# Optimization experiments

Hardware: AMD Instinct MI355X
Metric: run time of the kernel (lower is better)

## Reference

```python
import jax, jax.numpy as jnp
import numpy as np

EPS = 1e-12  # tf.nn.l2_normalize epsilon used by keras Dot(normalize=True)

def setup_inputs() -> dict:
    key = jax.random.key(0)
    k1, k2 = jax.random.split(key)
    a = jax.random.normal(k1, (16, 4096, 256), dtype=jnp.float32)
    b = jax.random.normal(k2, (16, 4096, 256), dtype=jnp.float32)
    return {"a": a, "b": b}

def _l2_normalize(x, axis=-1):
    # matches tf.nn.l2_normalize: x * rsqrt(max(sum(x^2), eps))
    sq = jnp.sum(x * x, axis=axis, keepdims=True)
    return x * jax.lax.rsqrt(jnp.maximum(sq, EPS))

def reference(a, b):
    # Original: full [B,N,N] cosine-similarity matrix then diag_part.
    # The diagonal equals the rowwise cosine similarity, computed directly.
    an = _l2_normalize(a, axis=2)  # [B, N, D]
    bn = _l2_normalize(b, axis=2)  # [B, N, D]
    return jnp.sum(an * bn, axis=2)  # [B, N]
```

## Files before the change

### kernel.cpp

```cpp
#include <hip/hip_runtime.h>


#define D 256
#define EPS 1e-12f

__global__ __launch_bounds__(256) void cosine_rows_kernel(
    const float* __restrict__ a,
    const float* __restrict__ b,
    float* __restrict__ out,
    int n_rows)
{
    const int lane = threadIdx.x & 63;
    const int wave = threadIdx.x >> 6;
    const int sub  = lane & 15;
    const int grp  = lane >> 4;
    const int row  = blockIdx.x * 16 + wave * 4 + grp;
    if (row >= n_rows) return;

    const float4* a4 = reinterpret_cast<const float4*>(a + (size_t)row * D);
    const float4* b4 = reinterpret_cast<const float4*>(b + (size_t)row * D);

    float4 av0 = a4[sub];
    float4 av1 = a4[sub + 16];
    float4 av2 = a4[sub + 32];
    float4 av3 = a4[sub + 48];
    float4 bv0 = b4[sub];
    float4 bv1 = b4[sub + 16];
    float4 bv2 = b4[sub + 32];
    float4 bv3 = b4[sub + 48];

    float sa = 0.f, sb = 0.f, sab = 0.f;
    #define ACC(av, bv)                                          \
        sa  += av.x*av.x + av.y*av.y + av.z*av.z + av.w*av.w;    \
        sb  += bv.x*bv.x + bv.y*bv.y + bv.z*bv.z + bv.w*bv.w;    \
        sab += av.x*bv.x + av.y*bv.y + av.z*bv.z + av.w*bv.w;
    ACC(av0, bv0)
    ACC(av1, bv1)
    ACC(av2, bv2)
    ACC(av3, bv3)
    #undef ACC

    #pragma unroll
    for (int off = 8; off > 0; off >>= 1) {
        sa  += __shfl_xor(sa,  off, 16);
        sb  += __shfl_xor(sb,  off, 16);
        sab += __shfl_xor(sab, off, 16);
    }

    if (sub == 0) {
        out[row] = sab * rsqrtf(fmaxf(sa, EPS)) * rsqrtf(fmaxf(sb, EPS));
    }
}

extern "C" void kernel_launch(void* const* d_in, const int* in_sizes, int n_in,
                              void* d_out, int out_size, void* d_ws, size_t ws_size,
                              hipStream_t stream)
{
    const float* a = (const float*)d_in[0];
    const float* b = (const float*)d_in[1];
    float* out = (float*)d_out;

    const int n_rows = out_size;
    const int rows_per_block = 16;
    const int grid = (n_rows + rows_per_block - 1) / rows_per_block;

    cosine_rows_kernel<<<grid, 256, 0, stream>>>(a, b, out, n_rows);
}
```

Baseline: 141.3 us.

## Split cosine row reduction into partial-sum and shuffle-reduce kernels

Splits the single fused kernel into two launches. The first computes per-thread partial sums of a·a, b·b and a·b and writes them to workspace. The second reloads those partials, does the 16-lane shuffle reduction and writes the normalized dot product. This adds a second launch plus an extra write and read of three partial arrays (3×16 floats per row), probably to test whether separating the reduction helps. The accumulation also switches to explicit fmaf chains.

```diff
diff --git a/kernel.cpp b/kernel.cpp
--- a/kernel.cpp
+++ b/kernel.cpp
@@ -1,44 +1,58 @@
 #include <hip/hip_runtime.h>
 
 
-#define D 256
 #define EPS 1e-12f
 
-__global__ __launch_bounds__(256) void cosine_rows_kernel(
-    const float* __restrict__ a,
-    const float* __restrict__ b,
-    float* __restrict__ out,
-    int n_rows)
+__global__ __launch_bounds__(256) void cosine_phase1(
+    const float4* __restrict__ a4,
+    const float4* __restrict__ b4,
+    float* __restrict__ ws_sa,
+    float* __restrict__ ws_sb,
+    float* __restrict__ ws_sab,
+    int n_part)
 {
-    const int lane = threadIdx.x & 63;
-    const int wave = threadIdx.x >> 6;
-    const int sub  = lane & 15;
-    const int grp  = lane >> 4;
-    const int row  = blockIdx.x * 16 + wave * 4 + grp;
-    if (row >= n_rows) return;
+    const int g = blockIdx.x * 256 + threadIdx.x;
+    if (g >= n_part) return;
+    const int row = g >> 4;
+    const int sub = g & 15;
 
-    const float4* a4 = reinterpret_cast<const float4*>(a + (size_t)row * D);
-    const float4* b4 = reinterpret_cast<const float4*>(b + (size_t)row * D);
+    const float4* __restrict__ ar = a4 + (size_t)row * 64 + sub;
+    const float4* __restrict__ br = b4 + (size_t)row * 64 + sub;
 
-    float4 av0 = a4[sub];
-    float4 av1 = a4[sub + 16];
-    float4 av2 = a4[sub + 32];
-    float4 av3 = a4[sub + 48];
-    float4 bv0 = b4[sub];
-    float4 bv1 = b4[sub + 16];
-    float4 bv2 = b4[sub + 32];
-    float4 bv3 = b4[sub + 48];
+    float4 av0 = ar[0],  av1 = ar[16], av2 = ar[32], av3 = ar[48];
+    float4 bv0 = br[0],  bv1 = br[16], bv2 = br[32], bv3 = br[48];
 
     float sa = 0.f, sb = 0.f, sab = 0.f;
-    #define ACC(av, bv)                                          \
-        sa  += av.x*av.x + av.y*av.y + av.z*av.z + av.w*av.w;    \
-        sb  += bv.x*bv.x + bv.y*bv.y + bv.z*bv.z + bv.w*bv.w;    \
-        sab += av.x*bv.x + av.y*bv.y + av.z*bv.z + av.w*bv.w;
+    #define ACC(av, bv)                                                       \
+        sa  = fmaf(av.x, av.x, fmaf(av.y, av.y, fmaf(av.z, av.z, fmaf(av.w, av.w, sa))));   \
+        sb  = fmaf(bv.x, bv.x, fmaf(bv.y, bv.y, fmaf(bv.z, bv.z, fmaf(bv.w, bv.w, sb))));   \
+        sab = fmaf(av.x, bv.x, fmaf(av.y, bv.y, fmaf(av.z, bv.z, fmaf(av.w, bv.w, sab))));
     ACC(av0, bv0)
     ACC(av1, bv1)
     ACC(av2, bv2)
     ACC(av3, bv3)
     #undef ACC
+
+    ws_sa[g]  = sa;
+    ws_sb[g]  = sb;
+    ws_sab[g] = sab;
+}
+
+__global__ __launch_bounds__(256) void cosine_phase2(
+    const float* __restrict__ ws_sa,
+    const float* __restrict__ ws_sb,
+    const float* __restrict__ ws_sab,
+    float* __restrict__ out,
+    int n_part)
+{
+    const int g = blockIdx.x * 256 + threadIdx.x;
+    if (g >= n_part) return;
+    const int sub = g & 15;
+    const int row = g >> 4;
+
+    float sa  = ws_sa[g];
+    float sb  = ws_sb[g];
+    float sab = ws_sab[g];
 
     #pragma unroll
     for (int off = 8; off > 0; off >>= 1) {
@@ -47,22 +61,26 @@
         sab += __shfl_xor(sab, off, 16);
     }
 
-    if (sub == 0) {
+    if (sub == 0)
         out[row] = sab * rsqrtf(fmaxf(sa, EPS)) * rsqrtf(fmaxf(sb, EPS));
-    }
 }
 
 extern "C" void kernel_launch(void* const* d_in, const int* in_sizes, int n_in,
                               void* d_out, int out_size, void* d_ws, size_t ws_size,
                               hipStream_t stream)
 {
-    const float* a = (const float*)d_in[0];
-    const float* b = (const float*)d_in[1];
+    const float4* a4 = (const float4*)d_in[0];
+    const float4* b4 = (const float4*)d_in[1];
     float* out = (float*)d_out;
 
     const int n_rows = out_size;
-    const int rows_per_block = 16;
-    const int grid = (n_rows + rows_per_block - 1) / rows_per_block;
+    const int n_part = n_rows * 16;
 
-    cosine_rows_kernel<<<grid, 256, 0, stream>>>(a, b, out, n_rows);
+    float* ws_sa  = (float*)d_ws;
+    float* ws_sb  = ws_sa + n_part;
+    float* ws_sab = ws_sb + n_part;
+
+    const int grid = (n_part + 255) / 256;
+    cosine_phase1<<<grid, 256, 0, stream>>>(a4, b4, ws_sa, ws_sb, ws_sab, n_part);
+    cosine_phase2<<<grid, 256, 0, stream>>>(ws_sa, ws_sb, ws_sab, out, n_part);
 }
```

After: 147.1 us. 4.1% more time.
